# Optimization experiments

Measured on AMD Instinct MI355X. Metric: run time of the kernel, lower is better.

Reference implementation:

```python
import jax, jax.numpy as jnp
import numpy as np

T, B, I, H, A = 2048, 2, 40, 44, 262144  # seq_len, batch, input, hidden, max action len
E = 2 * H  # 88, branch embedding dim; E + I == 128 (Linear in_features)


def setup_inputs() -> dict:
    key = jax.random.key(0)
    ks = jax.random.split(key, 11)
    s = 1.0 / np.sqrt(H).astype(np.float32)
    u = lambda k, shape: jax.random.uniform(k, shape, jnp.float32, -s, s)
    sl = 1.0 / np.sqrt(E + I).astype(np.float32)
    return {
        "x": jax.random.normal(ks[0], (T, B, I), jnp.float32),
        "h0": jax.random.normal(ks[1], (1, B, H), jnp.float32),
        "c0": jax.random.normal(ks[2], (1, B, H), jnp.float32),
        "action": jax.random.normal(ks[3], (B, A, I), jnp.float32),
        "act_length": jax.random.randint(ks[4], (B,), 1, A + 1, jnp.int32),
        "W_ih": u(ks[5], (4 * H, I)),
        "W_hh": u(ks[6], (4 * H, H)),
        "b_ih": u(ks[7], (4 * H,)),
        "b_hh": u(ks[8], (4 * H,)),
        "W_v": jax.random.uniform(ks[9], (1, E + I), jnp.float32, -sl, sl),
        "b_v": jax.random.uniform(ks[10], (1,), jnp.float32, -sl, sl),
    }


def _lstm_final(x, h0, c0, W_ih, W_hh, b_ih, b_hh):
    # single-layer LSTM, returns final (h, c), each (B, H); torch gate order i,f,g,o
    def step(carry, xt):
        h, c = carry
        g = xt @ W_ih.T + b_ih + h @ W_hh.T + b_hh  # (B, 4H)
        i, f, gg, o = jnp.split(g, 4, axis=-1)
        c = jax.nn.sigmoid(f) * c + jax.nn.sigmoid(i) * jnp.tanh(gg)
        h = jax.nn.sigmoid(o) * jnp.tanh(c)
        return (h, c), None
    (h, c), _ = jax.lax.scan(step, (h0[0], c0[0]), x)
    return h, c


def reference(x, h0, c0, action, act_length, W_ih, W_hh, b_ih, b_hh, W_v, b_v):
    h, c = _lstm_final(x, h0, c0, W_ih, W_hh, b_ih, b_hh)
    emb = jnp.concatenate([h, c], axis=-1)  # (B, 88) == brench_embeding[0]
    w = W_v[0]
    w_e, w_a = w[:E], w[E:]  # split Linear(128->1) weight over [embed | act]
    # val[b, i] = emb[b].w_e + action[b, i].w_a + b_v  (fused ragged linear)
    vals = (emb @ w_e)[:, None] + jnp.einsum("bad,d->ba", action, w_a) + b_v[0]
    mask = jnp.arange(A)[None, :] < act_length[:, None]  # ragged lengths
    return jnp.where(mask, vals, 0.0)
```

## Files before the change

### kernel.cpp

```cpp
#include <hip/hip_runtime.h>

typedef float v2f __attribute__((ext_vector_type(2)));
typedef float v4f __attribute__((ext_vector_type(4)));

#define T_STEPS 2048
#define BATCH   2
#define IDIM    40
#define HDIM    44
#define GDIM    176
#define ADIM    262144
#define EDIM    88
#define NEG_L   (-1.4426950408889634f)
#define NEG_2L  (-2.8853900817779268f)
#define NACT_BLK 4096

__global__ __launch_bounds__(192) void xproj_kernel(
    const float* __restrict__ x,
    const float* __restrict__ W_ih,
    const float* __restrict__ b_ih,
    const float* __restrict__ b_hh,
    float* __restrict__ xproj)
{
    const int tb = blockIdx.x;
    const int gi = threadIdx.x;
    __shared__ __align__(16) float xs[IDIM];
    if (threadIdx.x < IDIM) xs[threadIdx.x] = x[(size_t)tb * IDIM + threadIdx.x];
    __syncthreads();
    if (gi < GDIM) {
        const float* wr = W_ih + gi * IDIM;
        float a0 = 0.f, a1 = 0.f;
        #pragma unroll
        for (int i = 0; i < IDIM; i += 4) {
            float4 wv = *(const float4*)&wr[i];
            float4 xv = *(const float4*)&xs[i];
            a0 += wv.x * xv.x + wv.z * xv.z;
            a1 += wv.y * xv.y + wv.w * xv.w;
        }
        const float scale = (gi >= 2 * HDIM && gi < 3 * HDIM) ? NEG_2L : NEG_L;
        xproj[(size_t)tb * GDIM + gi] = scale * (a0 + a1 + b_ih[gi] + b_hh[gi]);
    }
}

__global__ __launch_bounds__(128)
__attribute__((amdgpu_waves_per_eu(1, 1)))
void lstm_action_kernel(
    const float* __restrict__ xproj,
    const float* __restrict__ h0,
    const float* __restrict__ c0,
    const float* __restrict__ W_hh,
    const float* __restrict__ W_v,
    const float* __restrict__ b_v,
    float* __restrict__ base_out,
    const float* __restrict__ action,
    float* __restrict__ out)
{
    if (blockIdx.x >= BATCH) {
        const int idx = (blockIdx.x - BATCH) * 128 + threadIdx.x;
        const float* row = action + (size_t)idx * IDIM;
        float a0 = 0.f, a1 = 0.f;
        #pragma unroll
        for (int i = 0; i < IDIM; i += 4) {
            float4 av = *(const float4*)&row[i];
            a0 += av.x * W_v[EDIM + i + 0] + av.z * W_v[EDIM + i + 2];
            a1 += av.y * W_v[EDIM + i + 1] + av.w * W_v[EDIM + i + 3];
        }
        out[idx] = a0 + a1;
        return;
    }

    const int b    = blockIdx.x;
    const int tid  = threadIdx.x;
    const int wave = tid >> 6;
    const int lane = tid & 63;
    const int sub  = lane & 31;
    const int half = lane >> 5;
    const bool act = (sub < 22);
    const int subc = act ? sub : 21;
    const int unit = wave * 22 + subc;

    __shared__ __align__(16) float hsh[2][64];
    __shared__ float part[2];

    const int row0 = half ? (2 * HDIM + unit) : unit;
    const int row1 = row0 + HDIM;
    const float sc0 = half ? NEG_2L : NEG_L;
    const float sc1 = NEG_L;

    v2f w0[22], w1[22];
    {
        const float* r0p = W_hh + (size_t)row0 * HDIM;
        const float* r1p = W_hh + (size_t)row1 * HDIM;
        #pragma unroll
        for (int k = 0; k < 22; ++k) {
            w0[k] = ((const v2f*)r0p)[k] * sc0;
            w1[k] = ((const v2f*)r1p)[k] * sc1;
        }
    }

    float c = c0[b * HDIM + unit];
    if (tid < HDIM) hsh[0][tid] = h0[b * HDIM + tid];
    if (tid >= HDIM && tid < 64) hsh[0][tid] = 0.f;
    __syncthreads();

    v2f hp[22];
    #pragma unroll
    for (int k = 0; k < 11; ++k) {
        v4f t = ((const v4f*)hsh[0])[k];
        hp[2 * k]     = __builtin_shufflevector(t, t, 0, 1);
        hp[2 * k + 1] = __builtin_shufflevector(t, t, 2, 3);
    }

    const float* xp = xproj + (size_t)b * GDIM;
    #define LDX(d0, d1, s) { const float* _a = xp + (size_t)(s) * (BATCH * GDIM); \
        d0 = _a[row0]; d1 = _a[row1]; }
    float r0v, r1v, p0v, p1v;
    LDX(r0v, r1v, 0) LDX(p0v, p1v, 1)

    float hval = 0.f;

    #define STEP(WB, NS) { \
        v2f a0 = {r0v, 0.f}, a1 = {r1v, 0.f}; \
        _Pragma("unroll") \
        for (int k = 0; k < 22; ++k) { \
            a0 = __builtin_elementwise_fma(w0[k], hp[k], a0); \
            a1 = __builtin_elementwise_fma(w1[k], hp[k], a1); \
        } \
        float y0 = a0.x + a0.y; \
        float y1 = a1.x + a1.y; \
        float v0 = __builtin_amdgcn_rcpf(1.0f + __builtin_amdgcn_exp2f(y0)); \
        float v1 = __builtin_amdgcn_rcpf(1.0f + __builtin_amdgcn_exp2f(y1)); \
         \
         \
        float sx1 = v0, sy1 = v1; \
        asm("v_permlane32_swap_b32 %0, %1" : "+v"(sx1), "+v"(sy1)); \
        float sx2 = v1, sy2 = v0; \
        asm("v_permlane32_swap_b32 %0, %1" : "+v"(sx2), "+v"(sy2)); \
        float s_i = half ? sx2 : v0; \
        float s_f = half ? sx1 : v1; \
        float w_g = half ? v0 : sy1; \
        float s_o = half ? v1 : sy2; \
        float t_g = __builtin_fmaf(2.0f, w_g, -1.0f); \
        c = s_f * c + s_i * t_g; \
        float w_c = __builtin_amdgcn_rcpf(1.0f + __builtin_amdgcn_exp2f(c * NEG_2L)); \
        hval = __builtin_fmaf(s_o + s_o, w_c, -s_o); \
        hsh[WB][unit] = hval; \
        __syncthreads(); \
        _Pragma("unroll") \
        for (int k = 0; k < 11; ++k) { \
            v4f t = ((const v4f*)hsh[WB])[k]; \
            hp[2 * k]     = __builtin_shufflevector(t, t, 0, 1); \
            hp[2 * k + 1] = __builtin_shufflevector(t, t, 2, 3); \
        } \
        r0v = p0v; r1v = p1v; \
        const int _ns = ((NS) < T_STEPS) ? (NS) : (T_STEPS - 1); \
        LDX(p0v, p1v, _ns) \
    }

    #pragma unroll 1
    for (int step = 0; step < T_STEPS; step += 2) {
        STEP(1, step + 2)
        STEP(0, step + 3)
    }
    #undef STEP
    #undef LDX

    float p = 0.f;
    if (act && half == 0) p = hval * W_v[unit] + c * W_v[HDIM + unit];
    #pragma unroll
    for (int off = 32; off; off >>= 1) p += __shfl_down(p, off);
    if (lane == 0) part[wave] = p;
    __syncthreads();
    if (tid == 0) base_out[b] = part[0] + part[1] + b_v[0];
}

__global__ __launch_bounds__(256) void finalize_kernel(
    const int*   __restrict__ act_length,
    const float* __restrict__ base,
    float* __restrict__ out)
{
    const int idx = blockIdx.x * 256 + threadIdx.x;
    const int b = idx >> 18;
    const int a = idx & (ADIM - 1);
    const float v = out[idx];
    out[idx] = (a < act_length[b]) ? v + base[b] : 0.f;
}

extern "C" void kernel_launch(void* const* d_in, const int* in_sizes, int n_in,
                              void* d_out, int out_size, void* d_ws, size_t ws_size,
                              hipStream_t stream) {
    const float* x        = (const float*)d_in[0];
    const float* h0       = (const float*)d_in[1];
    const float* c0       = (const float*)d_in[2];
    const float* action   = (const float*)d_in[3];
    const int*   act_len  = (const int*)  d_in[4];
    const float* W_ih     = (const float*)d_in[5];
    const float* W_hh     = (const float*)d_in[6];
    const float* b_ih     = (const float*)d_in[7];
    const float* b_hh     = (const float*)d_in[8];
    const float* W_v      = (const float*)d_in[9];
    const float* b_v      = (const float*)d_in[10];
    float* out = (float*)d_out;

    float* xproj = (float*)d_ws;
    float* base  = xproj + (size_t)T_STEPS * BATCH * GDIM;

    xproj_kernel<<<dim3(T_STEPS * BATCH), dim3(192), 0, stream>>>(
        x, W_ih, b_ih, b_hh, xproj);
    lstm_action_kernel<<<dim3(BATCH + NACT_BLK), dim3(128), 0, stream>>>(
        xproj, h0, c0, W_hh, W_v, b_v, base, action, out);
    finalize_kernel<<<dim3((BATCH * ADIM) / 256), dim3(256), 0, stream>>>(
        act_len, base, out);
}
```

Before: 565.1 us.

## Split LSTM hidden-state exchange into own-wave and foreign-wave halves around barrier

Weights and hidden-state registers are split into the half produced by the thread's own wave and the half produced by the other wave. The shared-memory layout is padded to 32 floats per wave. Each wave reads its own half of h before the barrier and the other wave's half after it, and the recurrent matvec does the own-half FMAs first. The aim is to shorten the serial critical path of each timestep by overlapping LDS reads with the barrier wait. Correctness now depends on a hand-placed s_waitcnt lgkmcnt(6) and on wave-level write/read visibility without a full sync.

```diff
diff --git a/kernel.cpp b/kernel.cpp
--- a/kernel.cpp
+++ b/kernel.cpp
@@ -86,29 +86,42 @@
     const float sc0 = half ? NEG_2L : NEG_L;
     const float sc1 = NEG_L;
 
-    v2f w0[22], w1[22];
+    const int ownb  = wave * 22;
+    const int forb  = (wave ^ 1) * 22;
+    const int wslot = wave * 32;
+    const int fbase = (wave ^ 1) * 32;
+
+    v2f w0o[11], w0f[11], w1o[11], w1f[11];
     {
         const float* r0p = W_hh + (size_t)row0 * HDIM;
         const float* r1p = W_hh + (size_t)row1 * HDIM;
         #pragma unroll
-        for (int k = 0; k < 22; ++k) {
-            w0[k] = ((const v2f*)r0p)[k] * sc0;
-            w1[k] = ((const v2f*)r1p)[k] * sc1;
+        for (int k = 0; k < 11; ++k) {
+            w0o[k] = ((const v2f*)(r0p + ownb))[k] * sc0;
+            w0f[k] = ((const v2f*)(r0p + forb))[k] * sc0;
+            w1o[k] = ((const v2f*)(r1p + ownb))[k] * sc1;
+            w1f[k] = ((const v2f*)(r1p + forb))[k] * sc1;
         }
     }
 
     float c = c0[b * HDIM + unit];
-    if (tid < HDIM) hsh[0][tid] = h0[b * HDIM + tid];
-    if (tid >= HDIM && tid < 64) hsh[0][tid] = 0.f;
-    __syncthreads();
-
-    v2f hp[22];
-    #pragma unroll
-    for (int k = 0; k < 11; ++k) {
-        v4f t = ((const v4f*)hsh[0])[k];
-        hp[2 * k]     = __builtin_shufflevector(t, t, 0, 1);
-        hp[2 * k + 1] = __builtin_shufflevector(t, t, 2, 3);
-    }
+
+    if (tid < HDIM) hsh[0][(tid / 22) * 32 + (tid % 22)] = h0[b * HDIM + tid];
+    __syncthreads();
+    v2f hO[11], hF[11];
+    {
+        const v4f* ob = (const v4f*)&hsh[0][wslot];
+        const v4f* fb = (const v4f*)&hsh[0][fbase];
+        #pragma unroll
+        for (int k = 0; k < 11; ++k) {
+            v4f oq = ob[k >> 1], fq = fb[k >> 1];
+            hO[k] = (k & 1) ? __builtin_shufflevector(oq, oq, 2, 3)
+                            : __builtin_shufflevector(oq, oq, 0, 1);
+            hF[k] = (k & 1) ? __builtin_shufflevector(fq, fq, 2, 3)
+                            : __builtin_shufflevector(fq, fq, 0, 1);
+        }
+    }
+    __syncthreads();
 
     const float* xp = xproj + (size_t)b * GDIM;
     #define LDX(d0, d1, s) { const float* _a = xp + (size_t)(s) * (BATCH * GDIM); \
@@ -119,17 +132,23 @@
     float hval = 0.f;
 
     #define STEP(WB, NS) { \
+         \
         v2f a0 = {r0v, 0.f}, a1 = {r1v, 0.f}; \
         _Pragma("unroll") \
-        for (int k = 0; k < 22; ++k) { \
-            a0 = __builtin_elementwise_fma(w0[k], hp[k], a0); \
-            a1 = __builtin_elementwise_fma(w1[k], hp[k], a1); \
+        for (int k = 0; k < 11; ++k) { \
+            a0 = __builtin_elementwise_fma(w0o[k], hO[k], a0); \
+            a1 = __builtin_elementwise_fma(w1o[k], hO[k], a1); \
+        } \
+         \
+        _Pragma("unroll") \
+        for (int k = 0; k < 11; ++k) { \
+            a0 = __builtin_elementwise_fma(w0f[k], hF[k], a0); \
+            a1 = __builtin_elementwise_fma(w1f[k], hF[k], a1); \
         } \
         float y0 = a0.x + a0.y; \
         float y1 = a1.x + a1.y; \
         float v0 = __builtin_amdgcn_rcpf(1.0f + __builtin_amdgcn_exp2f(y0)); \
         float v1 = __builtin_amdgcn_rcpf(1.0f + __builtin_amdgcn_exp2f(y1)); \
-         \
          \
         float sx1 = v0, sy1 = v1; \
         asm("v_permlane32_swap_b32 %0, %1" : "+v"(sx1), "+v"(sy1)); \
@@ -143,13 +162,31 @@
         c = s_f * c + s_i * t_g; \
         float w_c = __builtin_amdgcn_rcpf(1.0f + __builtin_amdgcn_exp2f(c * NEG_2L)); \
         hval = __builtin_fmaf(s_o + s_o, w_c, -s_o); \
-        hsh[WB][unit] = hval; \
-        __syncthreads(); \
-        _Pragma("unroll") \
-        for (int k = 0; k < 11; ++k) { \
-            v4f t = ((const v4f*)hsh[WB])[k]; \
-            hp[2 * k]     = __builtin_shufflevector(t, t, 0, 1); \
-            hp[2 * k + 1] = __builtin_shufflevector(t, t, 2, 3); \
+         \
+        hsh[WB][wslot + subc] = hval; \
+        { \
+            const v4f* ob = (const v4f*)&hsh[WB][wslot]; \
+            _Pragma("unroll") \
+            for (int k = 0; k < 11; ++k) { \
+                v4f oq = ob[k >> 1]; \
+                hO[k] = (k & 1) ? __builtin_shufflevector(oq, oq, 2, 3) \
+                                : __builtin_shufflevector(oq, oq, 0, 1); \
+            } \
+        } \
+         \
+        asm volatile("s_waitcnt lgkmcnt(6)" ::: "memory"); \
+        __builtin_amdgcn_sched_barrier(0); \
+        __builtin_amdgcn_s_barrier(); \
+        __builtin_amdgcn_sched_barrier(0); \
+         \
+        { \
+            const v4f* fb = (const v4f*)&hsh[WB][fbase]; \
+            _Pragma("unroll") \
+            for (int k = 0; k < 11; ++k) { \
+                v4f fq = fb[k >> 1]; \
+                hF[k] = (k & 1) ? __builtin_shufflevector(fq, fq, 2, 3) \
+                                : __builtin_shufflevector(fq, fq, 0, 1); \
+            } \
         } \
         r0v = p0v; r1v = p1v; \
         const int _ns = ((NS) < T_STEPS) ? (NS) : (T_STEPS - 1); \
```

After: 574.9 us. About the same (+1.7%).
